# Kernel tuning notes

Hardware: AMD Instinct MI355X
Metric: run time of the kernel (lower is better)

The kernel has to match this reference:

```python
import jax, jax.numpy as jnp
import numpy as np
import math

B, N, D_MODEL = 1, 2925, 1536
NUM_HEADS, HEAD_DIM = 12, 128
F, H, W = 13, 15, 15
MAX_SEQ = 1024
EPS = 1e-6


def _make_freqs(max_seq, dim):
    # (cos, sin) pairs for half-dim rotary frequencies, base 10000
    inv = 1.0 / (10000.0 ** (np.arange(0, dim, 2, dtype=np.float64) / dim))
    ang = np.arange(max_seq, dtype=np.float64)[:, None] * inv[None, :]
    return jnp.asarray(np.stack([np.cos(ang), np.sin(ang)], axis=-1), dtype=jnp.float32)


def setup_inputs() -> dict:
    key = jax.random.key(0)
    ks = jax.random.split(key, 10)
    s = 1.0 / math.sqrt(D_MODEL)
    dim_base = HEAD_DIM // 6              # 21
    dim_t = HEAD_DIM - 4 * dim_base       # 44
    dim_h = 2 * dim_base                  # 42
    return {
        "x": jax.random.normal(ks[0], (B, N, D_MODEL), dtype=jnp.float32),
        "Wq": jax.random.normal(ks[1], (D_MODEL, D_MODEL), dtype=jnp.float32) * s,
        "bq": jnp.zeros((D_MODEL,), dtype=jnp.float32),
        "Wk": jax.random.normal(ks[2], (D_MODEL, D_MODEL), dtype=jnp.float32) * s,
        "bk": jnp.zeros((D_MODEL,), dtype=jnp.float32),
        "Wv": jax.random.normal(ks[3], (D_MODEL, D_MODEL), dtype=jnp.float32) * s,
        "bv": jnp.zeros((D_MODEL,), dtype=jnp.float32),
        "Wo": jax.random.normal(ks[4], (D_MODEL, D_MODEL), dtype=jnp.float32) * s,
        "bo": jnp.zeros((D_MODEL,), dtype=jnp.float32),
        "q_scale": jnp.ones((D_MODEL,), dtype=jnp.float32),
        "k_scale": jnp.ones((D_MODEL,), dtype=jnp.float32),
        "freqs_t": _make_freqs(MAX_SEQ, dim_t),
        "freqs_h": _make_freqs(MAX_SEQ, dim_h),
        "freqs_w": _make_freqs(MAX_SEQ, dim_h),
        "f": F, "h": H, "w": W,
    }


def _rms_norm(x, scale, eps=EPS):
    var = jnp.mean(jnp.square(x), axis=-1, keepdims=True)
    return x * jax.lax.rsqrt(var + eps) * scale


def _rope_apply(x, f, h, w, freqs_t, freqs_h, freqs_w):
    # x: [b, n, H, D] with n == f*h*w
    b, n, nh, d = x.shape
    db = d // 6
    dt, dh, dw = d - 4 * db, 2 * db, 2 * db
    ft = jnp.broadcast_to(freqs_t[:f, None, None, :, :], (f, h, w, dt // 2, 2))
    fh = jnp.broadcast_to(freqs_h[None, :h, None, :, :], (f, h, w, dh // 2, 2))
    fw = jnp.broadcast_to(freqs_w[None, None, :w, :, :], (f, h, w, dw // 2, 2))
    fg = jnp.concatenate([ft, fh, fw], axis=3).reshape(n, d // 2, 2)[None, :, None, :, :]
    xc = x.reshape(b, n, nh, d // 2, 2)
    re = xc[..., 0] * fg[..., 0] - xc[..., 1] * fg[..., 1]
    im = xc[..., 0] * fg[..., 1] + xc[..., 1] * fg[..., 0]
    return jnp.stack([re, im], axis=-1).reshape(b, n, nh, d)


def reference(x, Wq, bq, Wk, bk, Wv, bv, Wo, bo, q_scale, k_scale,
              freqs_t, freqs_h, freqs_w, f, h, w):
    b, n, _ = x.shape
    nh, d = NUM_HEADS, HEAD_DIM
    # projections + RMSNorm across full hidden dim (before head split)
    q = _rms_norm(x @ Wq + bq, q_scale).reshape(b, n, nh, d)
    k = _rms_norm(x @ Wk + bk, k_scale).reshape(b, n, nh, d)
    v = (x @ Wv + bv).reshape(b, n, nh, d)
    # 3D RoPE on [b, n, H, D] layout
    q = _rope_apply(q, f, h, w, freqs_t, freqs_h, freqs_w)
    k = _rope_apply(k, f, h, w, freqs_t, freqs_h, freqs_w)
    # [b, H, n, d]
    q = q.transpose(0, 2, 1, 3)
    k = k.transpose(0, 2, 1, 3)
    v = v.transpose(0, 2, 1, 3)
    scores = jnp.einsum("bhid,bhjd->bhij", q, k) / math.sqrt(d)
    attn = jax.nn.softmax(scores, axis=-1)
    out = jnp.einsum("bhij,bhjd->bhid", attn, v)
    out = out.transpose(0, 2, 1, 3).reshape(b, n, nh * d)
    return out @ Wo + bo
```

## Files before the change

kernel.cpp:

```cpp
#include <hip/hip_runtime.h>


#define N_TOK 2925
#define DMODEL 1536
#define NHEAD 12
#define HDIM 128
#define KSPLIT 1472
#define VT_STRIDE 2944

typedef __attribute__((ext_vector_type(8))) __bf16 bf16x8;
typedef __attribute__((ext_vector_type(4))) float floatx4;

#define MFMA(a, b, c) __builtin_amdgcn_mfma_f32_16x16x32_bf16((a), (b), (c), 0, 0, 0)

static __device__ __forceinline__ unsigned short f2bf(float f) {
    unsigned u = __builtin_bit_cast(unsigned, f);
    return (unsigned short)((u + 0x7fffu + ((u >> 16) & 1u)) >> 16);
}

static __device__ __forceinline__ void gload_lds16(const unsigned short* g, unsigned short* l) {
    __builtin_amdgcn_global_load_lds((const __attribute__((address_space(1))) void*)g,
                                     (__attribute__((address_space(3))) void*)l, 16, 0, 0);
}

__global__ __launch_bounds__(256) void k_convert_x(const float* __restrict__ x,
                                                   unsigned short* __restrict__ xb, int n) {
    int i = (blockIdx.x * 256 + threadIdx.x) * 4;
    if (i < n) {
        float4 v = *(const float4*)(x + i);
        uint2 o;
        o.x = (unsigned)f2bf(v.x) | ((unsigned)f2bf(v.y) << 16);
        o.y = (unsigned)f2bf(v.z) | ((unsigned)f2bf(v.w) << 16);
        *(uint2*)(xb + i) = o;
    }
}

__global__ __launch_bounds__(256) void k_transpose_w(const float* __restrict__ W0,
                                                     const float* __restrict__ W1,
                                                     const float* __restrict__ W2,
                                                     const float* __restrict__ W3,
                                                     unsigned short* __restrict__ Wt) {
    __shared__ float tile[32][33];
    const float* W = blockIdx.z == 0 ? W0 : blockIdx.z == 1 ? W1 : blockIdx.z == 2 ? W2 : W3;
    unsigned short* out = Wt + (size_t)blockIdx.z * DMODEL * DMODEL;
    int tx = threadIdx.x, ty = threadIdx.y;
    int bx = blockIdx.x * 32, by = blockIdx.y * 32;
#pragma unroll
    for (int i = 0; i < 4; i++)
        tile[ty + 8 * i][tx] = W[(size_t)(by + ty + 8 * i) * DMODEL + bx + tx];
    __syncthreads();
#pragma unroll
    for (int i = 0; i < 4; i++)
        out[(size_t)(bx + ty + 8 * i) * DMODEL + by + tx] = f2bf(tile[tx][ty + 8 * i]);
}

__global__ __launch_bounds__(256, 2) void k_gemm(const unsigned short* __restrict__ A,
                                                 const unsigned short* __restrict__ BtBase,
                                                 const float* __restrict__ b0,
                                                 const float* __restrict__ b1,
                                                 const float* __restrict__ b2,
                                                 float* __restrict__ Cbase, int M) {
    const int z = blockIdx.z;
    const unsigned short* Bt = BtBase + (size_t)z * DMODEL * DMODEL;
    const float* bias = (z == 0) ? b0 : (z == 1) ? b1 : b2;
    float* C = Cbase + (size_t)z * M * DMODEL;

    __shared__ __align__(16) unsigned short As[128 * 32];
    __shared__ __align__(16) unsigned short Bs[128 * 32];

    const int tid = threadIdx.x;
    const int wave = tid >> 6, lane = tid & 63, quad = lane >> 4, l16 = lane & 15;
    const int wr = wave >> 1, wc = wave & 1;
    const int m0 = blockIdx.y * 128, n0 = blockIdx.x * 128;

    const int r4 = tid >> 2, c4 = (tid & 3) * 8;

    floatx4 acc[4][4] = {};

    for (int k0 = 0; k0 < DMODEL; k0 += 32) {
        gload_lds16(A + (size_t)(m0 + r4) * DMODEL + k0 + c4,       &As[r4 * 32 + c4]);
        gload_lds16(A + (size_t)(m0 + r4 + 64) * DMODEL + k0 + c4,  &As[(r4 + 64) * 32 + c4]);
        gload_lds16(Bt + (size_t)(n0 + r4) * DMODEL + k0 + c4,      &Bs[r4 * 32 + c4]);
        gload_lds16(Bt + (size_t)(n0 + r4 + 64) * DMODEL + k0 + c4, &Bs[(r4 + 64) * 32 + c4]);
        __syncthreads();

        bf16x8 af[4], bfm[4];
#pragma unroll
        for (int i = 0; i < 4; i++)
            af[i] = *(const bf16x8*)&As[(wr * 64 + i * 16 + l16) * 32 + quad * 8];
#pragma unroll
        for (int j = 0; j < 4; j++)
            bfm[j] = *(const bf16x8*)&Bs[(wc * 64 + j * 16 + l16) * 32 + quad * 8];
#pragma unroll
        for (int i = 0; i < 4; i++)
#pragma unroll
            for (int j = 0; j < 4; j++)
                acc[i][j] = MFMA(af[i], bfm[j], acc[i][j]);
        __syncthreads();
    }

#pragma unroll
    for (int j = 0; j < 4; j++) {
        int cg = n0 + wc * 64 + j * 16 + l16;
        float bv = bias[cg];
#pragma unroll
        for (int i = 0; i < 4; i++) {
            int rbase = m0 + wr * 64 + i * 16 + quad * 4;
#pragma unroll
            for (int r = 0; r < 4; r++) {
                int rg = rbase + r;
                if (rg < M) C[(size_t)rg * DMODEL + cg] = acc[i][j][r] + bv;
            }
        }
    }
}

__global__ __launch_bounds__(256) void k_norm_rope(const float* __restrict__ Qf,
                                                   const float* __restrict__ Kf,
                                                   const float* __restrict__ Vf,
                                                   const float* __restrict__ qsc,
                                                   const float* __restrict__ ksc,
                                                   const float* __restrict__ ft,
                                                   const float* __restrict__ fh,
                                                   const float* __restrict__ fw,
                                                   unsigned short* __restrict__ qb,
                                                   unsigned short* __restrict__ kb,
                                                   unsigned short* __restrict__ vb) {
    const int n = blockIdx.x;
    const int tid = threadIdx.x, wave = tid >> 6, lane = tid & 63;
    const int t_i = n / 225, rem = n % 225, h_i = rem / 15, w_i = rem % 15;
    const float att_scale = 0.08838834764831845f * 1.4426950408889634f;

    float2 qv[3], kv[3], vv[3];
    float sq = 0.f, sk = 0.f;
#pragma unroll
    for (int c = 0; c < 3; c++) {
        int p = tid + 256 * c;
        qv[c] = *(const float2*)(Qf + (size_t)n * DMODEL + 2 * p);
        kv[c] = *(const float2*)(Kf + (size_t)n * DMODEL + 2 * p);
        vv[c] = *(const float2*)(Vf + (size_t)n * DMODEL + 2 * p);
        sq += qv[c].x * qv[c].x + qv[c].y * qv[c].y;
        sk += kv[c].x * kv[c].x + kv[c].y * kv[c].y;
    }
#pragma unroll
    for (int off = 32; off >= 1; off >>= 1) {
        sq += __shfl_xor(sq, off, 64);
        sk += __shfl_xor(sk, off, 64);
    }
    __shared__ float red[2][4];
    if (lane == 0) { red[0][wave] = sq; red[1][wave] = sk; }
    __syncthreads();
    sq = red[0][0] + red[0][1] + red[0][2] + red[0][3];
    sk = red[1][0] + red[1][1] + red[1][2] + red[1][3];
    const float rq = rsqrtf(sq * (1.f / 1536.f) + 1e-6f) * att_scale;
    const float rk = rsqrtf(sk * (1.f / 1536.f) + 1e-6f);

#pragma unroll
    for (int c = 0; c < 3; c++) {
        int p = tid + 256 * c;
        int hd = p >> 6, pl = p & 63, dd = 2 * pl;
        float cs, sn;
        if (pl < 22)      { cs = ft[t_i * 44 + 2 * pl];        sn = ft[t_i * 44 + 2 * pl + 1]; }
        else if (pl < 43) { int pp = pl - 22; cs = fh[h_i * 42 + 2 * pp]; sn = fh[h_i * 42 + 2 * pp + 1]; }
        else              { int pp = pl - 43; cs = fw[w_i * 42 + 2 * pp]; sn = fw[w_i * 42 + 2 * pp + 1]; }
        int hidx = hd * 128 + dd;
        float q0 = qv[c].x * rq * qsc[hidx], q1 = qv[c].y * rq * qsc[hidx + 1];
        float k0 = kv[c].x * rk * ksc[hidx], k1 = kv[c].y * rk * ksc[hidx + 1];
        size_t o = ((size_t)hd * N_TOK + n) * HDIM + dd;
        unsigned qo = (unsigned)f2bf(q0 * cs - q1 * sn) | ((unsigned)f2bf(q0 * sn + q1 * cs) << 16);
        unsigned ko = (unsigned)f2bf(k0 * cs - k1 * sn) | ((unsigned)f2bf(k0 * sn + k1 * cs) << 16);
        unsigned vo = (unsigned)f2bf(vv[c].x) | ((unsigned)f2bf(vv[c].y) << 16);
        *(unsigned*)(qb + o) = qo;
        *(unsigned*)(kb + o) = ko;
        *(unsigned*)(vb + o) = vo;
    }
}

__global__ __launch_bounds__(256) void k_transpose_v(const unsigned short* __restrict__ vbi,
                                                     unsigned short* __restrict__ vt) {
    __shared__ unsigned short tile[32][33];
    const int head = blockIdx.z;
    const int t0 = blockIdx.x * 32, d0 = blockIdx.y * 32;
    const int tx = threadIdx.x, ty = threadIdx.y;
#pragma unroll
    for (int i = 0; i < 4; i++) {
        int t = t0 + ty + 8 * i;
        tile[ty + 8 * i][tx] = (t < N_TOK) ? vbi[((size_t)head * N_TOK + t) * HDIM + d0 + tx] : 0;
    }
    __syncthreads();
    int t = t0 + tx;
#pragma unroll
    for (int i = 0; i < 4; i++)
        vt[((size_t)head * HDIM + d0 + ty + 8 * i) * VT_STRIDE + t] = tile[tx][ty + 8 * i];
}

__global__ __launch_bounds__(256, 4) void k_attn_part(const unsigned short* __restrict__ qb,
                                                      const unsigned short* __restrict__ kb,
                                                      const unsigned short* __restrict__ vt,
                                                      float* __restrict__ Opart,
                                                      float* __restrict__ mbuf,
                                                      float* __restrict__ lbuf) {
    __shared__ __align__(16) unsigned short Ks[64 * 128];
    __shared__ __align__(16) unsigned short Vs[128 * 64];
    __shared__ __align__(16) unsigned short Ps[4][16 * 64];

    const int b = blockIdx.x + 46 * (blockIdx.y + 12 * (int)blockIdx.z);
    const int w = (b & 7) * 138 + (b >> 3);
    const int qblk = w % 46;
    const int head = (w / 46) % 12;
    const int z    = w / 552;

    const int tid = threadIdx.x, wave = tid >> 6, lane = tid & 63;
    const int quad = lane >> 4, l16 = lane & 15, x7 = l16 & 7;
    const int q0 = qblk * 64 + wave * 16;
    const unsigned short* qh = qb + (size_t)head * N_TOK * HDIM;
    const unsigned short* kh = kb + (size_t)head * N_TOK * HDIM;
    const unsigned short* vh = vt + (size_t)head * HDIM * VT_STRIDE;
    unsigned short* ps = Ps[wave];

    const int kbeg = z ? KSPLIT : 0;
    const int kend = z ? N_TOK : KSPLIT;
    const int ntile = (kend - kbeg + 63) >> 6;

    int koff[4];
#pragma unroll
    for (int ks = 0; ks < 4; ks++) {
        int c = ks * 4 + quad;
        koff[ks] = ((c & 8) | ((c & 7) ^ x7)) * 8;
    }
    const int pwq = (quad >> 1), pwh = (quad & 1) * 4;

    const int krow = tid >> 4, ksw = tid & 15;
    const int kc = (ksw & 8) | ((ksw & 7) ^ (krow & 7));
    const int vd = tid >> 3, vsw = tid & 7;
    const int vc = vsw ^ (vd & 7);
    const unsigned short* ksrc = kh + (size_t)krow * HDIM + kc * 8;
    const unsigned short* vsrc = vh + (size_t)vd * VT_STRIDE + vc * 8;

    bf16x8 aq[4];
    {
        int qrow = q0 + l16;
        if (qrow < N_TOK) {
#pragma unroll
            for (int ks = 0; ks < 4; ks++)
                aq[ks] = *(const bf16x8*)&qh[(size_t)qrow * HDIM + ks * 32 + quad * 8];
        } else {
#pragma unroll
            for (int ks = 0; ks < 4; ks++) aq[ks] = (bf16x8)(__bf16)0.0f;
        }
    }

    floatx4 oacc[8] = {};
    float m_l = -1e30f;
    float l_l = 0.f;

    {
        const bool part0 = (kbeg + 64 > kend);
        if (!part0) {
#pragma unroll
            for (int i = 0; i < 4; i++)
                gload_lds16(ksrc + (size_t)(kbeg + 16 * i) * HDIM, &Ks[(tid + 256 * i) * 8]);
        } else {
#pragma unroll
            for (int i = 0; i < 4; i++) {
                int gk = kbeg + krow + 16 * i;
                gk = gk < N_TOK ? gk : N_TOK - 1;
                gload_lds16(kh + (size_t)gk * HDIM + kc * 8, &Ks[(tid + 256 * i) * 8]);
            }
        }
#pragma unroll
        for (int i = 0; i < 4; i++)
            gload_lds16(vsrc + (size_t)(32 * i) * VT_STRIDE + kbeg, &Vs[(tid + 256 * i) * 8]);
    }

    for (int t = 0; t < ntile; t++) {
        const int kb0 = kbeg + t * 64;
        const bool fullt = (kb0 + 64 <= kend);
        const bool has_next = (t + 1 < ntile);

        asm volatile("s_waitcnt vmcnt(4)" ::: "memory");
        __builtin_amdgcn_sched_barrier(0);
        __builtin_amdgcn_s_barrier();

        floatx4 sa[4] = {};
        __builtin_amdgcn_s_setprio(1);
#pragma unroll
        for (int j = 0; j < 4; j++)
#pragma unroll
            for (int ks = 0; ks < 4; ks++) {
                bf16x8 bkf = *(const bf16x8*)&Ks[(j * 16 + l16) * HDIM + koff[ks]];
                sa[j] = MFMA(bkf, aq[ks], sa[j]);
            }
        __builtin_amdgcn_s_setprio(0);
        __builtin_amdgcn_s_barrier();

        if (has_next) {
            const int kn = kb0 + 64;
            if (kn + 64 <= kend) {
#pragma unroll
                for (int i = 0; i < 4; i++)
                    gload_lds16(ksrc + (size_t)(kn + 16 * i) * HDIM, &Ks[(tid + 256 * i) * 8]);
            } else {
#pragma unroll
                for (int i = 0; i < 4; i++) {
                    int gk = kn + krow + 16 * i;
                    gk = gk < N_TOK ? gk : N_TOK - 1;
                    gload_lds16(kh + (size_t)gk * HDIM + kc * 8, &Ks[(tid + 256 * i) * 8]);
                }
            }
        }

        float mt;
        if (fullt) {
            float m01 = fmaxf(fmaxf(sa[0][0], sa[0][1]), fmaxf(sa[0][2], sa[0][3]));
            float m23 = fmaxf(fmaxf(sa[1][0], sa[1][1]), fmaxf(sa[1][2], sa[1][3]));
            float m45 = fmaxf(fmaxf(sa[2][0], sa[2][1]), fmaxf(sa[2][2], sa[2][3]));
            float m67 = fmaxf(fmaxf(sa[3][0], sa[3][1]), fmaxf(sa[3][2], sa[3][3]));
            mt = fmaxf(fmaxf(m01, m23), fmaxf(m45, m67));
        } else {
            mt = -1e30f;
            const int kq = kb0 + quad * 4;
#pragma unroll
            for (int j = 0; j < 4; j++)
#pragma unroll
                for (int r = 0; r < 4; r++)
                    mt = fmaxf(mt, (kq + j * 16 + r < kend) ? sa[j][r] : -1e30f);
        }
        mt = fmaxf(mt, __shfl_xor(mt, 16));
        mt = fmaxf(mt, __shfl_xor(mt, 32));

        if (__any(mt > m_l + 8.f)) {
            float mn = fmaxf(m_l, mt);
            float alpha = exp2f(m_l - mn);
            m_l = mn;
            l_l *= alpha;
#pragma unroll
            for (int r = 0; r < 4; r++) {
                float ar = __shfl(alpha, quad * 4 + r, 16);
#pragma unroll
                for (int jd = 0; jd < 8; jd++) oacc[jd][r] *= ar;
            }
        }

        if (fullt) {
#pragma unroll
            for (int j = 0; j < 4; j++) {
                float p0 = exp2f(sa[j][0] - m_l), p1 = exp2f(sa[j][1] - m_l);
                float p2 = exp2f(sa[j][2] - m_l), p3 = exp2f(sa[j][3] - m_l);
                l_l += (p0 + p1) + (p2 + p3);
                uint2 wv;
                wv.x = (unsigned)__builtin_bit_cast(unsigned short, (__bf16)p0) |
                       ((unsigned)__builtin_bit_cast(unsigned short, (__bf16)p1) << 16);
                wv.y = (unsigned)__builtin_bit_cast(unsigned short, (__bf16)p2) |
                       ((unsigned)__builtin_bit_cast(unsigned short, (__bf16)p3) << 16);
                *(uint2*)&ps[l16 * 64 + (((j * 2 + pwq) ^ x7) << 3) + pwh] = wv;
            }
        } else {
            const int kq = kb0 + quad * 4;
#pragma unroll
            for (int j = 0; j < 4; j++) {
                float p[4];
#pragma unroll
                for (int r = 0; r < 4; r++) {
                    p[r] = (kq + j * 16 + r < kend) ? exp2f(sa[j][r] - m_l) : 0.f;
                    l_l += p[r];
                }
                uint2 wv;
                wv.x = (unsigned)__builtin_bit_cast(unsigned short, (__bf16)p[0]) |
                       ((unsigned)__builtin_bit_cast(unsigned short, (__bf16)p[1]) << 16);
                wv.y = (unsigned)__builtin_bit_cast(unsigned short, (__bf16)p[2]) |
                       ((unsigned)__builtin_bit_cast(unsigned short, (__bf16)p[3]) << 16);
                *(uint2*)&ps[l16 * 64 + (((j * 2 + pwq) ^ x7) << 3) + pwh] = wv;
            }
        }

        if (has_next) { asm volatile("s_waitcnt vmcnt(4)" ::: "memory"); }
        else          { asm volatile("s_waitcnt vmcnt(0)" ::: "memory"); }
        __builtin_amdgcn_sched_barrier(0);
        __builtin_amdgcn_s_barrier();

        __builtin_amdgcn_s_setprio(1);
#pragma unroll
        for (int ks = 0; ks < 2; ks++) {
            bf16x8 ap = *(const bf16x8*)&ps[l16 * 64 + koff[ks]];
#pragma unroll
            for (int jd = 0; jd < 8; jd++) {
                bf16x8 bvf = *(const bf16x8*)&Vs[(jd * 16 + l16) * 64 + koff[ks]];
                oacc[jd] = MFMA(ap, bvf, oacc[jd]);
            }
        }
        __builtin_amdgcn_s_setprio(0);
        __builtin_amdgcn_s_barrier();

        if (has_next) {
            const int kn = kb0 + 64;
#pragma unroll
            for (int i = 0; i < 4; i++)
                gload_lds16(vsrc + (size_t)(32 * i) * VT_STRIDE + kn, &Vs[(tid + 256 * i) * 8]);
        }
    }

    l_l += __shfl_xor(l_l, 16);
    l_l += __shfl_xor(l_l, 32);

#pragma unroll
    for (int r = 0; r < 4; r++) {
        int rg = q0 + quad * 4 + r;
        if (rg < N_TOK) {
            size_t rbase = ((size_t)(z * NHEAD + head) * N_TOK + rg) * HDIM;
#pragma unroll
            for (int jd = 0; jd < 8; jd++)
                Opart[rbase + jd * 16 + l16] = oacc[jd][r];
        }
    }
    if (quad == 0 && q0 + l16 < N_TOK) {
        int mi = (z * NHEAD + head) * N_TOK + q0 + l16;
        mbuf[mi] = m_l;
        lbuf[mi] = l_l;
    }
}

__global__ __launch_bounds__(256) void k_combine(const float* __restrict__ Opart,
                                                 const float* __restrict__ mbuf,
                                                 const float* __restrict__ lbuf,
                                                 unsigned short* __restrict__ ab) {
    const int R = NHEAD * N_TOK;
    int r = blockIdx.x * 8 + (threadIdx.x >> 5);
    if (r >= R) return;
    int l32 = threadIdx.x & 31;
    float m0 = mbuf[r], m1 = mbuf[R + r];
    float l0 = lbuf[r], l1 = lbuf[R + r];
    float m = fmaxf(m0, m1);
    float w0 = exp2f(m0 - m), w1 = exp2f(m1 - m);
    float inv = 1.f / (l0 * w0 + l1 * w1);
    w0 *= inv; w1 *= inv;
    float4 a = *(const float4*)&Opart[(size_t)r * HDIM + l32 * 4];
    float4 b = *(const float4*)&Opart[((size_t)R + r) * HDIM + l32 * 4];
    int head = r / N_TOK, tok = r % N_TOK;
    unsigned short* o = ab + (size_t)tok * DMODEL + head * HDIM + l32 * 4;
    uint2 pk;
    pk.x = (unsigned)f2bf(a.x * w0 + b.x * w1) | ((unsigned)f2bf(a.y * w0 + b.y * w1) << 16);
    pk.y = (unsigned)f2bf(a.z * w0 + b.z * w1) | ((unsigned)f2bf(a.w * w0 + b.w * w1) << 16);
    *(uint2*)o = pk;
}

extern "C" void kernel_launch(void* const* d_in, const int* in_sizes, int n_in,
                              void* d_out, int out_size, void* d_ws, size_t ws_size,
                              hipStream_t stream) {
    const float* x   = (const float*)d_in[0];
    const float* Wq  = (const float*)d_in[1];
    const float* bq  = (const float*)d_in[2];
    const float* Wk  = (const float*)d_in[3];
    const float* bk  = (const float*)d_in[4];
    const float* Wv  = (const float*)d_in[5];
    const float* bv  = (const float*)d_in[6];
    const float* Wo  = (const float*)d_in[7];
    const float* bo  = (const float*)d_in[8];
    const float* qsc = (const float*)d_in[9];
    const float* ksc = (const float*)d_in[10];
    const float* ft  = (const float*)d_in[11];
    const float* fh  = (const float*)d_in[12];
    const float* fw  = (const float*)d_in[13];

    char* ws = (char*)d_ws;
    unsigned short* xb   = (unsigned short*)ws; ws += (size_t)N_TOK * DMODEL * 2;
    unsigned short* Wt   = (unsigned short*)ws; ws += (size_t)4 * DMODEL * DMODEL * 2;
    unsigned short* ab   = (unsigned short*)ws; ws += (size_t)N_TOK * DMODEL * 2;
    char* qkvf_region    = ws;                  ws += (size_t)3 * N_TOK * DMODEL * 4;
    unsigned short* qkvb = (unsigned short*)ws; ws += (size_t)3 * N_TOK * DMODEL * 2;

    float* Qf = (float*)qkvf_region;
    float* Kf = Qf + (size_t)N_TOK * DMODEL;
    float* Vf = Qf + (size_t)2 * N_TOK * DMODEL;
    float* Opart = (float*)qkvf_region;
    float* mbuf  = Opart + (size_t)2 * NHEAD * N_TOK * HDIM;
    float* lbuf  = mbuf + (size_t)2 * NHEAD * N_TOK;
    unsigned short* vtp = (unsigned short*)(lbuf + (size_t)2 * NHEAD * N_TOK);

    unsigned short* qbp = qkvb;
    unsigned short* kbp = qkvb + (size_t)N_TOK * DMODEL;
    unsigned short* vbp = qkvb + (size_t)2 * N_TOK * DMODEL;

    const int nelem = N_TOK * DMODEL;
    k_convert_x<<<(nelem / 4 + 255) / 256, 256, 0, stream>>>(x, xb, nelem);
    k_transpose_w<<<dim3(48, 48, 4), dim3(32, 8), 0, stream>>>(Wq, Wk, Wv, Wo, Wt);
    k_gemm<<<dim3(12, 23, 3), 256, 0, stream>>>(xb, Wt, bq, bk, bv, Qf, N_TOK);
    k_norm_rope<<<N_TOK, 256, 0, stream>>>(Qf, Kf, Vf, qsc, ksc, ft, fh, fw, qbp, kbp, vbp);
    k_transpose_v<<<dim3(92, 4, NHEAD), dim3(32, 8), 0, stream>>>(vbp, vtp);
    k_attn_part<<<dim3(46, NHEAD, 2), 256, 0, stream>>>(qbp, kbp, vtp, Opart, mbuf, lbuf);
    k_combine<<<(NHEAD * N_TOK + 7) / 8, 256, 0, stream>>>(Opart, mbuf, lbuf, ab);
    k_gemm<<<dim3(12, 23, 1), 256, 0, stream>>>(ab, Wt + (size_t)3 * DMODEL * DMODEL,
                                                bo, bo, bo, (float*)d_out, N_TOK);
}
```

Measured before the change: 368.2 us.

## Process two 16-row query tiles per wave in attention with 128-thread blocks

The attention kernel now runs 2 waves per block instead of 4, and each wave handles 32 query rows as two 16-row tiles with separate accumulators and softmax state. Each K and V fragment read from LDS is reused for two MFMAs, which halves LDS read traffic per unit of compute and gives more independent MFMA chains. The tile loads are spread over 128 threads with 8 loads each, and the waitcnt thresholds are adjusted to match. The cost is roughly doubled register pressure (launch bounds drop to 128,2) and fewer waves per CU to hide latency.

```diff
diff --git a/kernel.cpp b/kernel.cpp
--- a/kernel.cpp
+++ b/kernel.cpp
@@ -194,7 +194,7 @@
         vt[((size_t)head * HDIM + d0 + ty + 8 * i) * VT_STRIDE + t] = tile[tx][ty + 8 * i];
 }
 
-__global__ __launch_bounds__(256, 4) void k_attn_part(const unsigned short* __restrict__ qb,
+__global__ __launch_bounds__(128, 2) void k_attn_part(const unsigned short* __restrict__ qb,
                                                       const unsigned short* __restrict__ kb,
                                                       const unsigned short* __restrict__ vt,
                                                       float* __restrict__ Opart,
@@ -202,7 +202,7 @@
                                                       float* __restrict__ lbuf) {
     __shared__ __align__(16) unsigned short Ks[64 * 128];
     __shared__ __align__(16) unsigned short Vs[128 * 64];
-    __shared__ __align__(16) unsigned short Ps[4][16 * 64];
+    __shared__ __align__(16) unsigned short Ps[2][2][16 * 64];
 
     const int b = blockIdx.x + 46 * (blockIdx.y + 12 * (int)blockIdx.z);
     const int w = (b & 7) * 138 + (b >> 3);
@@ -212,11 +212,12 @@
 
     const int tid = threadIdx.x, wave = tid >> 6, lane = tid & 63;
     const int quad = lane >> 4, l16 = lane & 15, x7 = l16 & 7;
-    const int q0 = qblk * 64 + wave * 16;
+    const int q0w = qblk * 64 + wave * 32;
     const unsigned short* qh = qb + (size_t)head * N_TOK * HDIM;
     const unsigned short* kh = kb + (size_t)head * N_TOK * HDIM;
     const unsigned short* vh = vt + (size_t)head * HDIM * VT_STRIDE;
-    unsigned short* ps = Ps[wave];
+    unsigned short* ps0 = Ps[wave][0];
+    unsigned short* ps1 = Ps[wave][1];
 
     const int kbeg = z ? KSPLIT : 0;
     const int kend = z ? N_TOK : KSPLIT;
@@ -230,47 +231,56 @@
     }
     const int pwq = (quad >> 1), pwh = (quad & 1) * 4;
 
-    const int krow = tid >> 4, ksw = tid & 15;
-    const int kc = (ksw & 8) | ((ksw & 7) ^ (krow & 7));
-    const int vd = tid >> 3, vsw = tid & 7;
-    const int vc = vsw ^ (vd & 7);
-    const unsigned short* ksrc = kh + (size_t)krow * HDIM + kc * 8;
-    const unsigned short* vsrc = vh + (size_t)vd * VT_STRIDE + vc * 8;
-
-    bf16x8 aq[4];
+    const int krow0 = tid >> 4, ksw = tid & 15;
+    const int kc = (ksw & 8) | ((ksw & 7) ^ (krow0 & 7));
+    const int vd0 = tid >> 3, vsw = tid & 7;
+    const int vc = vsw ^ (vd0 & 7);
+    const unsigned short* ksrc = kh + (size_t)krow0 * HDIM + kc * 8;
+    const unsigned short* vsrc = vh + (size_t)vd0 * VT_STRIDE + vc * 8;
+
+    bf16x8 aq0[4], aq1[4];
     {
-        int qrow = q0 + l16;
+        int qrow = q0w + l16;
         if (qrow < N_TOK) {
 #pragma unroll
             for (int ks = 0; ks < 4; ks++)
-                aq[ks] = *(const bf16x8*)&qh[(size_t)qrow * HDIM + ks * 32 + quad * 8];
+                aq0[ks] = *(const bf16x8*)&qh[(size_t)qrow * HDIM + ks * 32 + quad * 8];
         } else {
 #pragma unroll
-            for (int ks = 0; ks < 4; ks++) aq[ks] = (bf16x8)(__bf16)0.0f;
-        }
-    }
-
-    floatx4 oacc[8] = {};
-    float m_l = -1e30f;
-    float l_l = 0.f;
+            for (int ks = 0; ks < 4; ks++) aq0[ks] = (bf16x8)(__bf16)0.0f;
+        }
+        int qrow1 = q0w + 16 + l16;
+        if (qrow1 < N_TOK) {
+#pragma unroll
+            for (int ks = 0; ks < 4; ks++)
+                aq1[ks] = *(const bf16x8*)&qh[(size_t)qrow1 * HDIM + ks * 32 + quad * 8];
+        } else {
+#pragma unroll
+            for (int ks = 0; ks < 4; ks++) aq1[ks] = (bf16x8)(__bf16)0.0f;
+        }
+    }
+
+    floatx4 oacc0[8] = {}, oacc1[8] = {};
+    float m_l0 = -1e30f, m_l1 = -1e30f;
+    float l_l0 = 0.f, l_l1 = 0.f;
 
     {
         const bool part0 = (kbeg + 64 > kend);
         if (!part0) {
 #pragma unroll
-            for (int i = 0; i < 4; i++)
-                gload_lds16(ksrc + (size_t)(kbeg + 16 * i) * HDIM, &Ks[(tid + 256 * i) * 8]);
+            for (int i = 0; i < 8; i++)
+                gload_lds16(ksrc + (size_t)(kbeg + 8 * i) * HDIM, &Ks[(tid + 128 * i) * 8]);
         } else {
 #pragma unroll
-            for (int i = 0; i < 4; i++) {
-                int gk = kbeg + krow + 16 * i;
+            for (int i = 0; i < 8; i++) {
+                int gk = kbeg + krow0 + 8 * i;
                 gk = gk < N_TOK ? gk : N_TOK - 1;
-                gload_lds16(kh + (size_t)gk * HDIM + kc * 8, &Ks[(tid + 256 * i) * 8]);
-            }
-        }
-#pragma unroll
-        for (int i = 0; i < 4; i++)
-            gload_lds16(vsrc + (size_t)(32 * i) * VT_STRIDE + kbeg, &Vs[(tid + 256 * i) * 8]);
+                gload_lds16(kh + (size_t)gk * HDIM + kc * 8, &Ks[(tid + 128 * i) * 8]);
+            }
+        }
+#pragma unroll
+        for (int i = 0; i < 8; i++)
+            gload_lds16(vsrc + (size_t)(16 * i) * VT_STRIDE + kbeg, &Vs[(tid + 128 * i) * 8]);
     }
 
     for (int t = 0; t < ntile; t++) {
@@ -278,19 +288,23 @@
         const bool fullt = (kb0 + 64 <= kend);
         const bool has_next = (t + 1 < ntile);
 
-        asm volatile("s_waitcnt vmcnt(4)" ::: "memory");
+        asm volatile("s_waitcnt vmcnt(8)" ::: "memory");
         __builtin_amdgcn_sched_barrier(0);
         __builtin_amdgcn_s_barrier();
 
-        floatx4 sa[4] = {};
+        floatx4 sa0[4] = {}, sa1[4] = {};
         __builtin_amdgcn_s_setprio(1);
 #pragma unroll
-        for (int j = 0; j < 4; j++)
-#pragma unroll
-            for (int ks = 0; ks < 4; ks++) {
-                bf16x8 bkf = *(const bf16x8*)&Ks[(j * 16 + l16) * HDIM + koff[ks]];
-                sa[j] = MFMA(bkf, aq[ks], sa[j]);
-            }
+        for (int j = 0; j < 4; j++) {
+            bf16x8 bkf[4];
+#pragma unroll
+            for (int ks = 0; ks < 4; ks++)
+                bkf[ks] = *(const bf16x8*)&Ks[(j * 16 + l16) * HDIM + koff[ks]];
+#pragma unroll
+            for (int ks = 0; ks < 4; ks++) sa0[j] = MFMA(bkf[ks], aq0[ks], sa0[j]);
+#pragma unroll
+            for (int ks = 0; ks < 4; ks++) sa1[j] = MFMA(bkf[ks], aq1[ks], sa1[j]);
+        }
         __builtin_amdgcn_s_setprio(0);
         __builtin_amdgcn_s_barrier();
 
@@ -298,83 +312,117 @@
             const int kn = kb0 + 64;
             if (kn + 64 <= kend) {
 #pragma unroll
-                for (int i = 0; i < 4; i++)
-                    gload_lds16(ksrc + (size_t)(kn + 16 * i) * HDIM, &Ks[(tid + 256 * i) * 8]);
+                for (int i = 0; i < 8; i++)
+                    gload_lds16(ksrc + (size_t)(kn + 8 * i) * HDIM, &Ks[(tid + 128 * i) * 8]);
             } else {
 #pragma unroll
-                for (int i = 0; i < 4; i++) {
-                    int gk = kn + krow + 16 * i;
+                for (int i = 0; i < 8; i++) {
+                    int gk = kn + krow0 + 8 * i;
                     gk = gk < N_TOK ? gk : N_TOK - 1;
-                    gload_lds16(kh + (size_t)gk * HDIM + kc * 8, &Ks[(tid + 256 * i) * 8]);
+                    gload_lds16(kh + (size_t)gk * HDIM + kc * 8, &Ks[(tid + 128 * i) * 8]);
                 }
             }
         }
 
-        float mt;
+        float mt0, mt1;
         if (fullt) {
-            float m01 = fmaxf(fmaxf(sa[0][0], sa[0][1]), fmaxf(sa[0][2], sa[0][3]));
-            float m23 = fmaxf(fmaxf(sa[1][0], sa[1][1]), fmaxf(sa[1][2], sa[1][3]));
-            float m45 = fmaxf(fmaxf(sa[2][0], sa[2][1]), fmaxf(sa[2][2], sa[2][3]));
-            float m67 = fmaxf(fmaxf(sa[3][0], sa[3][1]), fmaxf(sa[3][2], sa[3][3]));
-            mt = fmaxf(fmaxf(m01, m23), fmaxf(m45, m67));
+            mt0 = fmaxf(fmaxf(fmaxf(fmaxf(sa0[0][0], sa0[0][1]), fmaxf(sa0[0][2], sa0[0][3])),
+                              fmaxf(fmaxf(sa0[1][0], sa0[1][1]), fmaxf(sa0[1][2], sa0[1][3]))),
+                        fmaxf(fmaxf(fmaxf(sa0[2][0], sa0[2][1]), fmaxf(sa0[2][2], sa0[2][3])),
+                              fmaxf(fmaxf(sa0[3][0], sa0[3][1]), fmaxf(sa0[3][2], sa0[3][3]))));
+            mt1 = fmaxf(fmaxf(fmaxf(fmaxf(sa1[0][0], sa1[0][1]), fmaxf(sa1[0][2], sa1[0][3])),
+                              fmaxf(fmaxf(sa1[1][0], sa1[1][1]), fmaxf(sa1[1][2], sa1[1][3]))),
+                        fmaxf(fmaxf(fmaxf(sa1[2][0], sa1[2][1]), fmaxf(sa1[2][2], sa1[2][3])),
+                              fmaxf(fmaxf(sa1[3][0], sa1[3][1]), fmaxf(sa1[3][2], sa1[3][3]))));
         } else {
-            mt = -1e30f;
+            mt0 = -1e30f; mt1 = -1e30f;
             const int kq = kb0 + quad * 4;
 #pragma unroll
             for (int j = 0; j < 4; j++)
 #pragma unroll
-                for (int r = 0; r < 4; r++)
-                    mt = fmaxf(mt, (kq + j * 16 + r < kend) ? sa[j][r] : -1e30f);
-        }
-        mt = fmaxf(mt, __shfl_xor(mt, 16));
-        mt = fmaxf(mt, __shfl_xor(mt, 32));
-
-        if (__any(mt > m_l + 8.f)) {
-            float mn = fmaxf(m_l, mt);
-            float alpha = exp2f(m_l - mn);
-            m_l = mn;
-            l_l *= alpha;
+                for (int r = 0; r < 4; r++) {
+                    bool v = (kq + j * 16 + r) < kend;
+                    mt0 = fmaxf(mt0, v ? sa0[j][r] : -1e30f);
+                    mt1 = fmaxf(mt1, v ? sa1[j][r] : -1e30f);
+                }
+        }
+        mt0 = fmaxf(mt0, __shfl_xor(mt0, 16));
+        mt0 = fmaxf(mt0, __shfl_xor(mt0, 32));
+        mt1 = fmaxf(mt1, __shfl_xor(mt1, 16));
+        mt1 = fmaxf(mt1, __shfl_xor(mt1, 32));
+
+        if (__any((mt0 > m_l0 + 8.f) || (mt1 > m_l1 + 8.f))) {
+            float mn0 = fmaxf(m_l0, mt0);
+            float a0 = exp2f(m_l0 - mn0);
+            m_l0 = mn0; l_l0 *= a0;
+            float mn1 = fmaxf(m_l1, mt1);
+            float a1 = exp2f(m_l1 - mn1);
+            m_l1 = mn1; l_l1 *= a1;
 #pragma unroll
             for (int r = 0; r < 4; r++) {
-                float ar = __shfl(alpha, quad * 4 + r, 16);
-#pragma unroll
-                for (int jd = 0; jd < 8; jd++) oacc[jd][r] *= ar;
+                float ar0 = __shfl(a0, quad * 4 + r, 16);
+                float ar1 = __shfl(a1, quad * 4 + r, 16);
+#pragma unroll
+                for (int jd = 0; jd < 8; jd++) {
+                    oacc0[jd][r] *= ar0;
+                    oacc1[jd][r] *= ar1;
+                }
             }
         }
 
         if (fullt) {
 #pragma unroll
             for (int j = 0; j < 4; j++) {
-                float p0 = exp2f(sa[j][0] - m_l), p1 = exp2f(sa[j][1] - m_l);
-                float p2 = exp2f(sa[j][2] - m_l), p3 = exp2f(sa[j][3] - m_l);
-                l_l += (p0 + p1) + (p2 + p3);
+                float p0 = exp2f(sa0[j][0] - m_l0), p1 = exp2f(sa0[j][1] - m_l0);
+                float p2 = exp2f(sa0[j][2] - m_l0), p3 = exp2f(sa0[j][3] - m_l0);
+                l_l0 += (p0 + p1) + (p2 + p3);
                 uint2 wv;
                 wv.x = (unsigned)__builtin_bit_cast(unsigned short, (__bf16)p0) |
                        ((unsigned)__builtin_bit_cast(unsigned short, (__bf16)p1) << 16);
                 wv.y = (unsigned)__builtin_bit_cast(unsigned short, (__bf16)p2) |
                        ((unsigned)__builtin_bit_cast(unsigned short, (__bf16)p3) << 16);
-                *(uint2*)&ps[l16 * 64 + (((j * 2 + pwq) ^ x7) << 3) + pwh] = wv;
+                *(uint2*)&ps0[l16 * 64 + (((j * 2 + pwq) ^ x7) << 3) + pwh] = wv;
+            }
+#pragma unroll
+            for (int j = 0; j < 4; j++) {
+                float p0 = exp2f(sa1[j][0] - m_l1), p1 = exp2f(sa1[j][1] - m_l1);
+                float p2 = exp2f(sa1[j][2] - m_l1), p3 = exp2f(sa1[j][3] - m_l1);
+                l_l1 += (p0 + p1) + (p2 + p3);
+                uint2 wv;
+                wv.x = (unsigned)__builtin_bit_cast(unsigned short, (__bf16)p0) |
+                       ((unsigned)__builtin_bit_cast(unsigned short, (__bf16)p1) << 16);
+                wv.y = (unsigned)__builtin_bit_cast(unsigned short, (__bf16)p2) |
+                       ((unsigned)__builtin_bit_cast(unsigned short, (__bf16)p3) << 16);
+                *(uint2*)&ps1[l16 * 64 + (((j * 2 + pwq) ^ x7) << 3) + pwh] = wv;
             }
         } else {
             const int kq = kb0 + quad * 4;
 #pragma unroll
             for (int j = 0; j < 4; j++) {
-                float p[4];
+                float p[4], q[4];
 #pragma unroll
                 for (int r = 0; r < 4; r++) {
-                    p[r] = (kq + j * 16 + r < kend) ? exp2f(sa[j][r] - m_l) : 0.f;
-                    l_l += p[r];
+                    bool v = (kq + j * 16 + r) < kend;
+                    p[r] = v ? exp2f(sa0[j][r] - m_l0) : 0.f;
+                    q[r] = v ? exp2f(sa1[j][r] - m_l1) : 0.f;
+                    l_l0 += p[r];
+                    l_l1 += q[r];
                 }
                 uint2 wv;
                 wv.x = (unsigned)__builtin_bit_cast(unsigned short, (__bf16)p[0]) |
                        ((unsigned)__builtin_bit_cast(unsigned short, (__bf16)p[1]) << 16);
                 wv.y = (unsigned)__builtin_bit_cast(unsigned short, (__bf16)p[2]) |
                        ((unsigned)__builtin_bit_cast(unsigned short, (__bf16)p[3]) << 16);
-                *(uint2*)&ps[l16 * 64 + (((j * 2 + pwq) ^ x7) << 3) + pwh] = wv;
-            }
-        }
-
-        if (has_next) { asm volatile("s_waitcnt vmcnt(4)" ::: "memory"); }
+                *(uint2*)&ps0[l16 * 64 + (((j * 2 + pwq) ^ x7) << 3) + pwh] = wv;
+                wv.x = (unsigned)__builtin_bit_cast(unsigned short, (__bf16)q[0]) |
+                       ((unsigned)__builtin_bit_cast(unsigned short, (__bf16)q[1]) << 16);
+                wv.y = (unsigned)__builtin_bit_cast(unsigned short, (__bf16)q[2]) |
+                       ((unsigned)__builtin_bit_cast(unsigned short, (__bf16)q[3]) << 16);
+                *(uint2*)&ps1[l16 * 64 + (((j * 2 + pwq) ^ x7) << 3) + pwh] = wv;
+            }
+        }
+
+        if (has_next) { asm volatile("s_waitcnt vmcnt(8)" ::: "memory"); }
         else          { asm volatile("s_waitcnt vmcnt(0)" ::: "memory"); }
         __builtin_amdgcn_sched_barrier(0);
         __builtin_amdgcn_s_barrier();
@@ -382,11 +430,13 @@
         __builtin_amdgcn_s_setprio(1);
 #pragma unroll
         for (int ks = 0; ks < 2; ks++) {
-            bf16x8 ap = *(const bf16x8*)&ps[l16 * 64 + koff[ks]];
+            bf16x8 ap0 = *(const bf16x8*)&ps0[l16 * 64 + koff[ks]];
+            bf16x8 ap1 = *(const bf16x8*)&ps1[l16 * 64 + koff[ks]];
 #pragma unroll
             for (int jd = 0; jd < 8; jd++) {
                 bf16x8 bvf = *(const bf16x8*)&Vs[(jd * 16 + l16) * 64 + koff[ks]];
-                oacc[jd] = MFMA(ap, bvf, oacc[jd]);
+                oacc0[jd] = MFMA(ap0, bvf, oacc0[jd]);
+                oacc1[jd] = MFMA(ap1, bvf, oacc1[jd]);
             }
         }
         __builtin_amdgcn_s_setprio(0);
@@ -395,28 +445,46 @@
         if (has_next) {
             const int kn = kb0 + 64;
 #pragma unroll
-            for (int i = 0; i < 4; i++)
-                gload_lds16(vsrc + (size_t)(32 * i) * VT_STRIDE + kn, &Vs[(tid + 256 * i) * 8]);
-        }
-    }
-
-    l_l += __shfl_xor(l_l, 16);
-    l_l += __shfl_xor(l_l, 32);
+            for (int i = 0; i < 8; i++)
+                gload_lds16(vsrc + (size_t)(16 * i) * VT_STRIDE + kn, &Vs[(tid + 128 * i) * 8]);
+        }
+    }
+
+    l_l0 += __shfl_xor(l_l0, 16);
+    l_l0 += __shfl_xor(l_l0, 32);
+    l_l1 += __shfl_xor(l_l1, 16);
+    l_l1 += __shfl_xor(l_l1, 32);
 
 #pragma unroll
     for (int r = 0; r < 4; r++) {
-        int rg = q0 + quad * 4 + r;
-        if (rg < N_TOK) {
-            size_t rbase = ((size_t)(z * NHEAD + head) * N_TOK + rg) * HDIM;
+        int rg0 = q0w + quad * 4 + r;
+        if (rg0 < N_TOK) {
+            size_t rbase = ((size_t)(z * NHEAD + head) * N_TOK + rg0) * HDIM;
 #pragma unroll
             for (int jd = 0; jd < 8; jd++)
-                Opart[rbase + jd * 16 + l16] = oacc[jd][r];
-        }
-    }
-    if (quad == 0 && q0 + l16 < N_TOK) {
-        int mi = (z * NHEAD + head) * N_TOK + q0 + l16;
-        mbuf[mi] = m_l;
-        lbuf[mi] = l_l;
+                Opart[rbase + jd * 16 + l16] = oacc0[jd][r];
+        }
+        int rg1 = q0w + 16 + quad * 4 + r;
+        if (rg1 < N_TOK) {
+            size_t rbase = ((size_t)(z * NHEAD + head) * N_TOK + rg1) * HDIM;
+#pragma unroll
+            for (int jd = 0; jd < 8; jd++)
+                Opart[rbase + jd * 16 + l16] = oacc1[jd][r];
+        }
+    }
+    if (quad == 0) {
+        int rg0 = q0w + l16;
+        if (rg0 < N_TOK) {
+            int mi = (z * NHEAD + head) * N_TOK + rg0;
+            mbuf[mi] = m_l0;
+            lbuf[mi] = l_l0;
+        }
+        int rg1 = q0w + 16 + l16;
+        if (rg1 < N_TOK) {
+            int mi = (z * NHEAD + head) * N_TOK + rg1;
+            mbuf[mi] = m_l1;
+            lbuf[mi] = l_l1;
+        }
     }
 }
 
@@ -487,7 +555,7 @@
     k_gemm<<<dim3(12, 23, 3), 256, 0, stream>>>(xb, Wt, bq, bk, bv, Qf, N_TOK);
     k_norm_rope<<<N_TOK, 256, 0, stream>>>(Qf, Kf, Vf, qsc, ksc, ft, fh, fw, qbp, kbp, vbp);
     k_transpose_v<<<dim3(92, 4, NHEAD), dim3(32, 8), 0, stream>>>(vbp, vtp);
-    k_attn_part<<<dim3(46, NHEAD, 2), 256, 0, stream>>>(qbp, kbp, vtp, Opart, mbuf, lbuf);
+    k_attn_part<<<dim3(46, NHEAD, 2), 128, 0, stream>>>(qbp, kbp, vtp, Opart, mbuf, lbuf);
     k_combine<<<(NHEAD * N_TOK + 7) / 8, 256, 0, stream>>>(Opart, mbuf, lbuf, ab);
     k_gemm<<<dim3(12, 23, 1), 256, 0, stream>>>(ab, Wt + (size_t)3 * DMODEL * DMODEL,
                                                 bo, bo, bo, (float*)d_out, N_TOK);
```

Measured after the change: 394.0 us. +7.0%, slower.
